# Optimization experiments

Hardware: AMD Instinct MI355X
Metric: run time of the kernel (lower is better)

Reference implementation:

```python
import jax, jax.numpy as jnp
import numpy as np

N_NODES = 80000
N_EDGES = 1280000
IN_DIM = 32
EDGE_DIM = 16
HID = 64
DEPTH = 4
BN_EPS = 1e-5
LN_EPS = 1e-5


def setup_inputs() -> dict:
    key = jax.random.key(0)
    ks = jax.random.split(key, 20)
    s = lambda fan: 1.0 / np.sqrt(fan)
    inp = {
        "x": jax.random.normal(ks[0], (N_NODES, IN_DIM), jnp.float32),
        "edge_index": jax.random.randint(ks[1], (2, N_EDGES), 0, N_NODES, jnp.int32),
        "edge_attr": jax.random.normal(ks[2], (N_EDGES, EDGE_DIM), jnp.float32),
        # input embeddings
        "Wx": jax.random.normal(ks[3], (IN_DIM, HID), jnp.float32) * s(IN_DIM),
        "bx": jnp.zeros((HID,), jnp.float32),
        "We": jax.random.normal(ks[4], (EDGE_DIM, HID), jnp.float32) * s(EDGE_DIM),
        "be": jnp.zeros((HID,), jnp.float32),
        # per-layer GIN MLP params (stacked over DEPTH)
        "W1": jax.random.normal(ks[5], (DEPTH, HID, 2 * HID), jnp.float32) * s(HID),
        "b1": jnp.zeros((DEPTH, 2 * HID), jnp.float32),
        "g1": jnp.ones((DEPTH, 2 * HID), jnp.float32),   # BatchNorm gamma
        "bt1": jnp.zeros((DEPTH, 2 * HID), jnp.float32),  # BatchNorm beta
        "W2": jax.random.normal(ks[6], (DEPTH, 2 * HID, HID), jnp.float32) * s(2 * HID),
        "b2": jnp.zeros((DEPTH, HID), jnp.float32),
        "eps": jnp.zeros((DEPTH,), jnp.float32),           # GIN epsilon, init 0
        # per-layer LayerNorm params
        "ln_g": jnp.ones((DEPTH, HID), jnp.float32),
        "ln_b": jnp.zeros((DEPTH, HID), jnp.float32),
    }
    return inp


def reference(x, edge_index, edge_attr, Wx, bx, We, be, W1, b1, g1, bt1, W2, b2, eps, ln_g, ln_b):
    n = x.shape[0]
    h = jax.nn.relu(x @ Wx + bx)                      # [N, HID]
    ea = jax.nn.relu(edge_attr @ We + be)             # [E, HID]
    row, col = edge_index[0], edge_index[1]           # source, target
    L = W1.shape[0]
    for l in range(L):
        # message: relu(x_j + edge_attr), scatter-add into target nodes
        msg = jax.nn.relu(h[row] + ea)                # [E, HID]
        agg = jax.ops.segment_sum(msg, col, num_segments=n)  # [N, HID]
        z = (1.0 + eps[l]) * h + agg
        # GIN MLP: Linear -> BatchNorm(train stats) -> ReLU -> Linear
        z = z @ W1[l] + b1[l]                         # [N, 2*HID]
        mu = z.mean(axis=0)
        var = z.var(axis=0)                           # biased, as torch BN training
        z = (z - mu) * jax.lax.rsqrt(var + BN_EPS) * g1[l] + bt1[l]
        z = jax.nn.relu(z)
        z = z @ W2[l] + b2[l]                         # [N, HID]
        # LayerNorm
        lm = z.mean(axis=-1, keepdims=True)
        lv = z.var(axis=-1, keepdims=True)
        z = (z - lm) * jax.lax.rsqrt(lv + LN_EPS) * ln_g[l] + ln_b[l]
        if l < L - 1:
            z = jax.nn.relu(z)
        h = z
    return h  # JK == 'last'
```

## Files before the change

### kernel.cpp

```cpp
#include <hip/hip_runtime.h>
#include <cstdint>

typedef _Float16 half8 __attribute__((ext_vector_type(8)));
typedef float f32x4 __attribute__((ext_vector_type(4)));

#define NNODES 80000
#define NEDGES 1280000
#define INDIM 32
#define EDIM 16
#define HID 64
#define HID2 128
#define DEPTH 4
#define BN_EPS 1e-5f
#define LN_EPS 1e-5f
#define NB 313
#define NPX 10000
#define EPS 10000

union U16x8 { uint4 v; _Float16 h[8]; };

__global__ __launch_bounds__(256) void k_node_embed(
    const float* __restrict__ x, const float* __restrict__ Wx,
    const float* __restrict__ bx, _Float16* __restrict__ h16) {
    int gw = (blockIdx.x * 256 + threadIdx.x) >> 6;
    int lane = threadIdx.x & 63;
    if (gw >= NNODES) return;
    float xv = (lane < INDIM) ? x[(size_t)gw * INDIM + lane] : 0.f;
    float acc = bx[lane];
#pragma unroll
    for (int k = 0; k < INDIM; k++)
        acc = fmaf(__shfl(xv, k, 64), Wx[k * HID + lane], acc);
    h16[(size_t)gw * HID + lane] = (_Float16)fmaxf(acc, 0.f);
}

__global__ __launch_bounds__(256) void k_prep(
    const float* __restrict__ W1, const float* __restrict__ W2,
    _Float16* __restrict__ w1T, _Float16* __restrict__ w2T) {
    int id = blockIdx.x * 256 + threadIdx.x;
    if (id < DEPTH * 128 * 64) {
        int l = id / 8192, r = id % 8192, n = r / 64, k = r % 64;
        w1T[id] = (_Float16)W1[(size_t)l * 8192 + k * 128 + n];
    } else {
        int idx = id - DEPTH * 128 * 64;
        int l = idx / 8192, r = idx % 8192, n = r / 128, k = r % 128;
        w2T[idx] = (_Float16)W2[(size_t)l * 8192 + k * 64 + n];
    }
}

__global__ __launch_bounds__(256) void k_hist(const int* __restrict__ col,
                                              int* __restrict__ deg) {
    int xcd = blockIdx.x & 7;
    int slice = blockIdx.x >> 3;
    int base = slice * EPS;
    int lo = xcd * NPX;
    const int4* c4 = (const int4*)(col + base);
    for (int i = threadIdx.x; i < EPS / 4; i += 256) {
        int4 c = c4[i];
#pragma unroll
        for (int u = 0; u < 4; u++) {
            int cc = (&c.x)[u];
            if ((unsigned)(cc - lo) < (unsigned)NPX) atomicAdd(&deg[cc], 1);
        }
    }
}

__global__ __launch_bounds__(256) void k_scan1(const int* __restrict__ deg, int* __restrict__ bsum) {
    __shared__ int s[256];
    int i = blockIdx.x * 256 + threadIdx.x;
    int v = (i < NNODES) ? deg[i] : 0;
    s[threadIdx.x] = v;
    __syncthreads();
    for (int o = 128; o > 0; o >>= 1) {
        if (threadIdx.x < o) s[threadIdx.x] += s[threadIdx.x + o];
        __syncthreads();
    }
    if (threadIdx.x == 0) bsum[blockIdx.x] = s[0];
}

__global__ __launch_bounds__(512) void k_scan2(const int* __restrict__ bsum, int* __restrict__ boff) {
    __shared__ int s[512];
    int t = threadIdx.x;
    s[t] = (t < NB) ? bsum[t] : 0;
    __syncthreads();
    for (int o = 1; o < 512; o <<= 1) {
        int v = (t >= o) ? s[t - o] : 0;
        __syncthreads();
        s[t] += v;
        __syncthreads();
    }
    if (t < NB) boff[t] = (t == 0) ? 0 : s[t - 1];
}

__global__ __launch_bounds__(256) void k_scan3(const int* __restrict__ deg,
                                               const int* __restrict__ boff,
                                               int* __restrict__ row_off) {
    __shared__ int s[256];
    int i = blockIdx.x * 256 + threadIdx.x;
    int t = threadIdx.x;
    int v = (i < NNODES) ? deg[i] : 0;
    s[t] = v;
    __syncthreads();
    for (int o = 1; o < 256; o <<= 1) {
        int u = (t >= o) ? s[t - o] : 0;
        __syncthreads();
        s[t] += u;
        __syncthreads();
    }
    int incl = s[t];
    if (i < NNODES) row_off[i] = boff[blockIdx.x] + incl - v;
    if (i == NNODES - 1) row_off[NNODES] = boff[blockIdx.x] + incl;
}

__global__ __launch_bounds__(256) void k_copy(const int* __restrict__ src, int* __restrict__ dst) {
    int i = blockIdx.x * 256 + threadIdx.x;
    if (i < NNODES) dst[i] = src[i];
}

__global__ __launch_bounds__(256) void k_scatter(
    const int* __restrict__ row, const int* __restrict__ col,
    int* __restrict__ cursor, uint2* __restrict__ sre) {
    int xcd = blockIdx.x & 7;
    int slice = blockIdx.x >> 3;
    int base = slice * EPS;
    int lo = xcd * NPX;
    const int4* c4 = (const int4*)(col + base);
    for (int i = threadIdx.x; i < EPS / 4; i += 256) {
        int4 c = c4[i];
        int e0 = base + i * 4;
#pragma unroll
        for (int u = 0; u < 4; u++) {
            int cc = (&c.x)[u];
            if ((unsigned)(cc - lo) < (unsigned)NPX) {
                int e = e0 + u;
                int pos = atomicAdd(&cursor[cc], 1);
                sre[pos] = make_uint2((unsigned)row[e], (unsigned)e);
            }
        }
    }
}

__global__ __launch_bounds__(256) void k_edge_embed(
    const float* __restrict__ eat, const uint2* __restrict__ sre,
    const float* __restrict__ We, const float* __restrict__ be,
    _Float16* __restrict__ eas, int* __restrict__ srow) {
    __shared__ __align__(16) unsigned char lds[4][8192];
    int tid = threadIdx.x;
    int w = tid >> 6, lane = tid & 63;
    unsigned char* A = lds[w];
    unsigned char* O = lds[w];
    int ebase = blockIdx.x * 256 + w * 64;
    int b = lane >> 4, c = lane & 15;
    half8 bf[4];
#pragma unroll
    for (int t = 0; t < 4; t++) {
        half8 v = {};
        if (b < 2) {
#pragma unroll
            for (int j = 0; j < 8; j++) {
                int k = b * 8 + j;
                v[j] = (_Float16)We[k * HID + t * 16 + c];
            }
        }
        bf[t] = v;
    }
    float bias[4];
#pragma unroll
    for (int t = 0; t < 4; t++) bias[t] = be[t * 16 + c];
    uint2 se = sre[ebase + lane];
    srow[ebase + lane] = (int)se.x;
    const float4* ar = (const float4*)(eat + (size_t)se.y * EDIM);
    float4 a0 = ar[0], a1 = ar[1], a2 = ar[2], a3 = ar[3];
    U16x8 lo, hi;
    lo.h[0] = (_Float16)a0.x; lo.h[1] = (_Float16)a0.y;
    lo.h[2] = (_Float16)a0.z; lo.h[3] = (_Float16)a0.w;
    lo.h[4] = (_Float16)a1.x; lo.h[5] = (_Float16)a1.y;
    lo.h[6] = (_Float16)a1.z; lo.h[7] = (_Float16)a1.w;
    hi.h[0] = (_Float16)a2.x; hi.h[1] = (_Float16)a2.y;
    hi.h[2] = (_Float16)a2.z; hi.h[3] = (_Float16)a2.w;
    hi.h[4] = (_Float16)a3.x; hi.h[5] = (_Float16)a3.y;
    hi.h[6] = (_Float16)a3.z; hi.h[7] = (_Float16)a3.w;
    *(uint4*)(A + lane * 80) = lo.v;
    *(uint4*)(A + lane * 80 + 16) = hi.v;
    __syncthreads();
    half8 af[4];
#pragma unroll
    for (int it = 0; it < 4; it++) {
        half8 z = {};
        af[it] = (b < 2) ? *(const half8*)(A + (it * 16 + c) * 80 + b * 16) : z;
    }
    __syncthreads();
#pragma unroll
    for (int it = 0; it < 4; it++) {
#pragma unroll
        for (int t = 0; t < 4; t++) {
            f32x4 acc = {0.f, 0.f, 0.f, 0.f};
            acc = __builtin_amdgcn_mfma_f32_16x16x32_f16(af[it], bf[t], acc, 0, 0, 0);
#pragma unroll
            for (int r = 0; r < 4; r++) {
                int erow = it * 16 + b * 4 + r;
                int chan = t * 16 + c;
                float v = fmaxf(acc[r] + bias[t], 0.f);
                int byteoff = (erow * 128 + chan * 2) ^ ((erow & 7) << 4);
                *(_Float16*)(O + byteoff) = (_Float16)v;
            }
        }
    }
    __syncthreads();
    uint4* dst = (uint4*)(eas + (size_t)(ebase + lane) * HID);
#pragma unroll
    for (int q = 0; q < 8; q++)
        dst[q] = *(const uint4*)(O + ((lane * 128 + q * 16) ^ ((lane & 7) << 4)));
}

__global__ __launch_bounds__(256) void k_msg(
    const _Float16* __restrict__ h16, const int* __restrict__ row_off,
    const int* __restrict__ srow, const _Float16* __restrict__ eas,
    const float* __restrict__ epsp, _Float16* __restrict__ zc16) {
    int gw = (blockIdx.x * 256 + threadIdx.x) >> 6;
    int lane = threadIdx.x & 63;
    if (gw >= NNODES) return;
    int beg = row_off[gw], end = row_off[gw + 1];
    float acc = 0.f;
    int e = beg;
    for (; e + 7 < end; e += 8) {
        int j[8];
#pragma unroll
        for (int u = 0; u < 8; u++) j[u] = srow[e + u];
        float hv[8], ev[8];
#pragma unroll
        for (int u = 0; u < 8; u++) hv[u] = (float)h16[(size_t)j[u] * HID + lane];
#pragma unroll
        for (int u = 0; u < 8; u++) ev[u] = (float)eas[(size_t)(e + u) * HID + lane];
        float t0 = fmaxf(hv[0] + ev[0], 0.f) + fmaxf(hv[1] + ev[1], 0.f);
        float t1 = fmaxf(hv[2] + ev[2], 0.f) + fmaxf(hv[3] + ev[3], 0.f);
        float t2 = fmaxf(hv[4] + ev[4], 0.f) + fmaxf(hv[5] + ev[5], 0.f);
        float t3 = fmaxf(hv[6] + ev[6], 0.f) + fmaxf(hv[7] + ev[7], 0.f);
        acc += (t0 + t1) + (t2 + t3);
    }
    for (; e < end; ++e) {
        int j = srow[e];
        float hv = (float)h16[(size_t)j * HID + lane];
        float ev = (float)eas[(size_t)e * HID + lane];
        acc += fmaxf(hv + ev, 0.f);
    }
    float epsl = *epsp;
    float hv0 = (float)h16[(size_t)gw * HID + lane];
    zc16[(size_t)gw * HID + lane] = (_Float16)((1.f + epsl) * hv0 + acc);
}

__global__ __launch_bounds__(256) void k_gemm1(
    const _Float16* __restrict__ zc16, const _Float16* __restrict__ w1Tl,
    const float* __restrict__ b1l, _Float16* __restrict__ z1,
    float* __restrict__ bn_acc) {
    __shared__ __align__(16) unsigned char At[64 * 128];
    __shared__ __align__(16) unsigned char Bt[128 * 128];
    __shared__ float red[4][HID2][2];
    int tid = threadIdx.x;
    int nb = blockIdx.x * 64;
#pragma unroll
    for (int i = 0; i < 2; i++) {
        int id = tid + 256 * i;
        int node = id >> 3, c = id & 7;
        uint4 v = *(const uint4*)(zc16 + (size_t)(nb + node) * HID + c * 8);
        *(uint4*)(At + node * 128 + ((c ^ (node & 7)) << 4)) = v;
    }
#pragma unroll
    for (int i = 0; i < 4; i++) {
        int id = tid + 256 * i;
        int r = id >> 3, c = id & 7;
        uint4 v = *(const uint4*)(w1Tl + (size_t)r * HID + c * 8);
        *(uint4*)(Bt + r * 128 + ((c ^ (r & 7)) << 4)) = v;
    }
    __syncthreads();
    int lane = tid & 63, w = tid >> 6;
    int rl = lane & 15, b = lane >> 4;
    f32x4 acc[8];
#pragma unroll
    for (int t = 0; t < 8; t++) acc[t] = (f32x4){0.f, 0.f, 0.f, 0.f};
#pragma unroll
    for (int s = 0; s < 2; s++) {
        int arow = w * 16 + rl;
        half8 af = *(const half8*)(At + arow * 128 + (((s * 4 + b) ^ (rl & 7)) << 4));
#pragma unroll
        for (int t = 0; t < 8; t++) {
            int brow = t * 16 + rl;
            half8 bf = *(const half8*)(Bt + brow * 128 + (((s * 4 + b) ^ (rl & 7)) << 4));
            acc[t] = __builtin_amdgcn_mfma_f32_16x16x32_f16(af, bf, acc[t], 0, 0, 0);
        }
    }
#pragma unroll
    for (int t = 0; t < 8; t++) {
        int colg = t * 16 + rl;
        float bias = b1l[colg];
        float s = 0.f, q = 0.f;
#pragma unroll
        for (int r = 0; r < 4; r++) {
            float v = acc[t][r] + bias;
            int node = nb + w * 16 + b * 4 + r;
            z1[(size_t)node * HID2 + colg] = (_Float16)v;
            s += v;
            q = fmaf(v, v, q);
        }
        s += __shfl_xor(s, 16, 64); s += __shfl_xor(s, 32, 64);
        q += __shfl_xor(q, 16, 64); q += __shfl_xor(q, 32, 64);
        if (b == 0) { red[w][colg][0] = s; red[w][colg][1] = q; }
    }
    __syncthreads();
    int ch = tid & 127, which = tid >> 7;
    float tot = red[0][ch][which] + red[1][ch][which] + red[2][ch][which] + red[3][ch][which];
    atomicAdd(&bn_acc[which * HID2 + ch], tot);
}

__global__ __launch_bounds__(256) void k_mlp2(
    const _Float16* __restrict__ z1, const float* __restrict__ bn_acc,
    const float* __restrict__ g1l, const float* __restrict__ bt1l,
    const _Float16* __restrict__ w2Tl, const float* __restrict__ b2l,
    const float* __restrict__ lngl, const float* __restrict__ lnbl,
    int last, _Float16* __restrict__ hout, float* __restrict__ fout) {
    __shared__ __align__(16) unsigned char Yt[64 * 256];
    __shared__ __align__(16) unsigned char Wt[64 * 256];
    __shared__ float sbn[256];
    int tid = threadIdx.x;
    int nb = blockIdx.x * 64;
    if (tid < HID2) {
        float inv_n = 1.f / (float)NNODES;
        float mu = bn_acc[tid] * inv_n;
        float ex2 = bn_acc[HID2 + tid] * inv_n;
        float rs = rsqrtf(ex2 - mu * mu + BN_EPS);
        float sc = g1l[tid] * rs;
        sbn[tid] = sc;
        sbn[HID2 + tid] = bt1l[tid] - mu * sc;
    }
#pragma unroll
    for (int i = 0; i < 4; i++) {
        int id = tid + 256 * i;
        int r = id >> 4, c = id & 15;
        uint4 v = *(const uint4*)(w2Tl + (size_t)r * HID2 + c * 8);
        *(uint4*)(Wt + r * 256 + ((c ^ (r & 7)) << 4)) = v;
    }
    __syncthreads();
#pragma unroll
    for (int i = 0; i < 4; i++) {
        int id = tid + 256 * i;
        int node = id >> 4, c = id & 15;
        U16x8 u, o;
        u.v = *(const uint4*)(z1 + (size_t)(nb + node) * HID2 + c * 8);
#pragma unroll
        for (int j = 0; j < 8; j++) {
            int chn = c * 8 + j;
            float y = fmaxf(fmaf((float)u.h[j], sbn[chn], sbn[HID2 + chn]), 0.f);
            o.h[j] = (_Float16)y;
        }
        *(uint4*)(Yt + node * 256 + ((c ^ (node & 7)) << 4)) = o.v;
    }
    __syncthreads();
    int lane = tid & 63, w = tid >> 6;
    int rl = lane & 15, b = lane >> 4;
    f32x4 acc[4];
#pragma unroll
    for (int t = 0; t < 4; t++) acc[t] = (f32x4){0.f, 0.f, 0.f, 0.f};
#pragma unroll
    for (int s = 0; s < 4; s++) {
        int arow = w * 16 + rl;
        half8 af = *(const half8*)(Yt + arow * 256 + (((s * 4 + b) ^ (rl & 7)) << 4));
#pragma unroll
        for (int t = 0; t < 4; t++) {
            int brow = t * 16 + rl;
            half8 bf = *(const half8*)(Wt + brow * 256 + (((s * 4 + b) ^ (rl & 7)) << 4));
            acc[t] = __builtin_amdgcn_mfma_f32_16x16x32_f16(af, bf, acc[t], 0, 0, 0);
        }
    }
    float a[4][4];
#pragma unroll
    for (int t = 0; t < 4; t++) {
        float bias = b2l[t * 16 + rl];
#pragma unroll
        for (int r = 0; r < 4; r++) a[r][t] = acc[t][r] + bias;
    }
    float m[4], vv[4];
#pragma unroll
    for (int r = 0; r < 4; r++) {
        float s = (a[r][0] + a[r][1]) + (a[r][2] + a[r][3]);
        s += __shfl_xor(s, 1, 64); s += __shfl_xor(s, 2, 64);
        s += __shfl_xor(s, 4, 64); s += __shfl_xor(s, 8, 64);
        m[r] = s * (1.f / 64.f);
    }
#pragma unroll
    for (int r = 0; r < 4; r++) {
        float t0 = a[r][0] - m[r], t1 = a[r][1] - m[r];
        float t2 = a[r][2] - m[r], t3 = a[r][3] - m[r];
        float q = (t0 * t0 + t1 * t1) + (t2 * t2 + t3 * t3);
        q += __shfl_xor(q, 1, 64); q += __shfl_xor(q, 2, 64);
        q += __shfl_xor(q, 4, 64); q += __shfl_xor(q, 8, 64);
        vv[r] = rsqrtf(q * (1.f / 64.f) + LN_EPS);
    }
#pragma unroll
    for (int t = 0; t < 4; t++) {
        int colg = t * 16 + rl;
        float lg = lngl[colg], lb = lnbl[colg];
#pragma unroll
        for (int r = 0; r < 4; r++) {
            float o = (a[r][t] - m[r]) * vv[r] * lg + lb;
            size_t node = nb + w * 16 + b * 4 + r;
            if (last) {
                fout[node * HID + colg] = o;
            } else {
                hout[node * HID + colg] = (_Float16)fmaxf(o, 0.f);
            }
        }
    }
}

extern "C" void kernel_launch(void* const* d_in, const int* in_sizes, int n_in,
                              void* d_out, int out_size, void* d_ws, size_t ws_size,
                              hipStream_t stream) {
    const float* x   = (const float*)d_in[0];
    const int*   ei  = (const int*)d_in[1];
    const float* eat = (const float*)d_in[2];
    const float* Wx  = (const float*)d_in[3];
    const float* bx  = (const float*)d_in[4];
    const float* We  = (const float*)d_in[5];
    const float* be  = (const float*)d_in[6];
    const float* W1  = (const float*)d_in[7];
    const float* b1  = (const float*)d_in[8];
    const float* g1  = (const float*)d_in[9];
    const float* bt1 = (const float*)d_in[10];
    const float* W2  = (const float*)d_in[11];
    const float* b2  = (const float*)d_in[12];
    const float* eps = (const float*)d_in[13];
    const float* lng = (const float*)d_in[14];
    const float* lnb = (const float*)d_in[15];
    const int* row = ei;
    const int* col = ei + NEDGES;

    char* p = (char*)d_ws;
    auto alloc = [&](size_t bytes) -> char* {
        char* r = p;
        p += (bytes + 255) & ~(size_t)255;
        return r;
    };
    _Float16* h16  = (_Float16*)alloc((size_t)NNODES * HID * 2);
    _Float16* zc16 = (_Float16*)alloc((size_t)NNODES * HID * 2);
    _Float16* z1   = (_Float16*)alloc((size_t)NNODES * HID2 * 2);
    int* row_off   = (int*)alloc((size_t)(NNODES + 1) * 4);
    uint2* sre     = (uint2*)alloc((size_t)NEDGES * 8);
    int* srow      = (int*)alloc((size_t)NEDGES * 4);
    _Float16* eas  = (_Float16*)alloc((size_t)NEDGES * HID * 2);
    _Float16* w1T  = (_Float16*)alloc((size_t)DEPTH * 128 * 64 * 2);
    _Float16* w2T  = (_Float16*)alloc((size_t)DEPTH * 64 * 128 * 2);
    float* bn_acc  = (float*)alloc(256 * 4);
    int* cursor = (int*)z1;
    int* bsum   = (int*)z1 + NNODES;
    int* boff   = bsum + NB;
    (void)ws_size; (void)in_sizes; (void)n_in; (void)out_size;

    hipMemsetAsync(cursor, 0, (size_t)NNODES * 4, stream);
    k_node_embed<<<(NNODES + 3) / 4, 256, 0, stream>>>(x, Wx, bx, h16);
    k_prep<<<(DEPTH * 8192 * 2) / 256, 256, 0, stream>>>(W1, W2, w1T, w2T);
    k_hist<<<(NEDGES / EPS) * 8, 256, 0, stream>>>(col, cursor);
    k_scan1<<<NB, 256, 0, stream>>>(cursor, bsum);
    k_scan2<<<1, 512, 0, stream>>>(bsum, boff);
    k_scan3<<<NB, 256, 0, stream>>>(cursor, boff, row_off);
    k_copy<<<NB, 256, 0, stream>>>(row_off, cursor);
    k_scatter<<<(NEDGES / EPS) * 8, 256, 0, stream>>>(row, col, cursor, sre);
    k_edge_embed<<<NEDGES / 256, 256, 0, stream>>>(eat, sre, We, be, eas, srow);

    const int msg_blocks = (NNODES + 3) / 4;
    const int mm_blocks = NNODES / 64;
    for (int l = 0; l < DEPTH; ++l) {
        k_msg<<<msg_blocks, 256, 0, stream>>>(h16, row_off, srow, eas, eps + l, zc16);
        hipMemsetAsync(bn_acc, 0, 256 * 4, stream);
        k_gemm1<<<mm_blocks, 256, 0, stream>>>(zc16, w1T + (size_t)l * 8192,
                                               b1 + (size_t)l * HID2, z1, bn_acc);
        k_mlp2<<<mm_blocks, 256, 0, stream>>>(z1, bn_acc,
                                              g1 + (size_t)l * HID2, bt1 + (size_t)l * HID2,
                                              w2T + (size_t)l * 8192,
                                              b2 + (size_t)l * HID,
                                              lng + (size_t)l * HID, lnb + (size_t)l * HID,
                                              (l == DEPTH - 1) ? 1 : 0, h16, (float*)d_out);
    }
}
```

Baseline: 688.9 us.

## Vectorize message gather with 16-byte loads and fold BN accumulator reset

Restructures the per-node aggregation so each wavefront processes 8 edges at once, with 8 lanes per edge each loading 16 bytes of fp16 features, instead of one 2-byte scalar load per lane per edge. Partial sums are combined with cross-lane shuffles before one vectorized store per node. The BatchNorm accumulator reset moves from a separate memset into the first block of the message kernel, saving one launch per layer. It costs extra shuffle reductions and a padded tail path that loads a clamped dummy edge.

```diff
diff --git a/kernel.cpp b/kernel.cpp
--- a/kernel.cpp
+++ b/kernel.cpp
@@ -215,37 +215,70 @@
 __global__ __launch_bounds__(256) void k_msg(
     const _Float16* __restrict__ h16, const int* __restrict__ row_off,
     const int* __restrict__ srow, const _Float16* __restrict__ eas,
-    const float* __restrict__ epsp, _Float16* __restrict__ zc16) {
+    const float* __restrict__ epsp, _Float16* __restrict__ zc16,
+    float* __restrict__ bn_acc) {
+    if (blockIdx.x == 0) bn_acc[threadIdx.x] = 0.f;
     int gw = (blockIdx.x * 256 + threadIdx.x) >> 6;
     int lane = threadIdx.x & 63;
     if (gw >= NNODES) return;
+    int grp = lane >> 3;
+    int c8 = (lane & 7) * 8;
     int beg = row_off[gw], end = row_off[gw + 1];
-    float acc = 0.f;
+    float a[8] = {0.f, 0.f, 0.f, 0.f, 0.f, 0.f, 0.f, 0.f};
     int e = beg;
-    for (; e + 7 < end; e += 8) {
-        int j[8];
-#pragma unroll
-        for (int u = 0; u < 8; u++) j[u] = srow[e + u];
-        float hv[8], ev[8];
-#pragma unroll
-        for (int u = 0; u < 8; u++) hv[u] = (float)h16[(size_t)j[u] * HID + lane];
-#pragma unroll
-        for (int u = 0; u < 8; u++) ev[u] = (float)eas[(size_t)(e + u) * HID + lane];
-        float t0 = fmaxf(hv[0] + ev[0], 0.f) + fmaxf(hv[1] + ev[1], 0.f);
-        float t1 = fmaxf(hv[2] + ev[2], 0.f) + fmaxf(hv[3] + ev[3], 0.f);
-        float t2 = fmaxf(hv[4] + ev[4], 0.f) + fmaxf(hv[5] + ev[5], 0.f);
-        float t3 = fmaxf(hv[6] + ev[6], 0.f) + fmaxf(hv[7] + ev[7], 0.f);
-        acc += (t0 + t1) + (t2 + t3);
-    }
-    for (; e < end; ++e) {
-        int j = srow[e];
-        float hv = (float)h16[(size_t)j * HID + lane];
-        float ev = (float)eas[(size_t)e * HID + lane];
-        acc += fmaxf(hv + ev, 0.f);
-    }
-    float epsl = *epsp;
-    float hv0 = (float)h16[(size_t)gw * HID + lane];
-    zc16[(size_t)gw * HID + lane] = (_Float16)((1.f + epsl) * hv0 + acc);
+    for (; e + 16 <= end; e += 16) {
+        int e0 = e + grp, e1 = e + 8 + grp;
+        int j0 = srow[e0], j1 = srow[e1];
+        U16x8 hv0, ev0, hv1, ev1;
+        hv0.v = *(const uint4*)(h16 + (size_t)j0 * HID + c8);
+        ev0.v = *(const uint4*)(eas + (size_t)e0 * HID + c8);
+        hv1.v = *(const uint4*)(h16 + (size_t)j1 * HID + c8);
+        ev1.v = *(const uint4*)(eas + (size_t)e1 * HID + c8);
+#pragma unroll
+        for (int q = 0; q < 8; q++) {
+            a[q] += fmaxf((float)hv0.h[q] + (float)ev0.h[q], 0.f) +
+                    fmaxf((float)hv1.h[q] + (float)ev1.h[q], 0.f);
+        }
+    }
+    for (; e + 8 <= end; e += 8) {
+        int e0 = e + grp;
+        int j0 = srow[e0];
+        U16x8 hv0, ev0;
+        hv0.v = *(const uint4*)(h16 + (size_t)j0 * HID + c8);
+        ev0.v = *(const uint4*)(eas + (size_t)e0 * HID + c8);
+#pragma unroll
+        for (int q = 0; q < 8; q++)
+            a[q] += fmaxf((float)hv0.h[q] + (float)ev0.h[q], 0.f);
+    }
+    if (e < end) {
+        int eidx = e + grp;
+        bool valid = eidx < end;
+        int ec = valid ? eidx : (NEDGES - 1);
+        int j = srow[ec];
+        U16x8 hv, ev;
+        hv.v = *(const uint4*)(h16 + (size_t)j * HID + c8);
+        ev.v = *(const uint4*)(eas + (size_t)ec * HID + c8);
+        if (valid) {
+#pragma unroll
+            for (int q = 0; q < 8; q++)
+                a[q] += fmaxf((float)hv.h[q] + (float)ev.h[q], 0.f);
+        }
+    }
+#pragma unroll
+    for (int q = 0; q < 8; q++) {
+        a[q] += __shfl_xor(a[q], 8, 64);
+        a[q] += __shfl_xor(a[q], 16, 64);
+        a[q] += __shfl_xor(a[q], 32, 64);
+    }
+    if (grp == 0) {
+        float epsl = 1.f + *epsp;
+        U16x8 h0, o;
+        h0.v = *(const uint4*)(h16 + (size_t)gw * HID + c8);
+#pragma unroll
+        for (int q = 0; q < 8; q++)
+            o.h[q] = (_Float16)(epsl * (float)h0.h[q] + a[q]);
+        *(uint4*)(zc16 + (size_t)gw * HID + c8) = o.v;
+    }
 }
 
 __global__ __launch_bounds__(256) void k_gemm1(
@@ -468,8 +501,7 @@
     const int msg_blocks = (NNODES + 3) / 4;
     const int mm_blocks = NNODES / 64;
     for (int l = 0; l < DEPTH; ++l) {
-        k_msg<<<msg_blocks, 256, 0, stream>>>(h16, row_off, srow, eas, eps + l, zc16);
-        hipMemsetAsync(bn_acc, 0, 256 * 4, stream);
+        k_msg<<<msg_blocks, 256, 0, stream>>>(h16, row_off, srow, eas, eps + l, zc16, bn_acc);
         k_gemm1<<<mm_blocks, 256, 0, stream>>>(zc16, w1T + (size_t)l * 8192,
                                                b1 + (size_t)l * HID2, z1, bn_acc);
         k_mlp2<<<mm_blocks, 256, 0, stream>>>(z1, bn_acc,
```

After: 627.5 us. 1.1x faster.
